# Optimization experiments

Measured on AMD Instinct MI355X. Metric: run time of the kernel, lower is better.

Reference implementation:

```python
import jax, jax.numpy as jnp
import numpy as np

N_NODES = 50000
N_EDGES = 640000
D_IN = 128
D_H1 = 128
D_H2 = 256
NEG_SLOPE = 0.2


def setup_inputs() -> dict:
    key = jax.random.key(0)
    ks = jax.random.split(key, 12)
    s = 1.0 / np.sqrt(D_IN)
    inp = {
        'x': jax.random.normal(ks[0], (N_NODES, D_IN), dtype=jnp.float32),
        'edge_index': jax.random.randint(ks[1], (2, N_EDGES), 0, N_NODES, dtype=jnp.int64),
        # GATv2 layer 1: 128 -> 128 (separate lin_l / lin_r, attention vec, residual proj, bias)
        'Wl1': jax.random.normal(ks[2], (D_IN, D_H1), dtype=jnp.float32) * s,
        'Wr1': jax.random.normal(ks[3], (D_IN, D_H1), dtype=jnp.float32) * s,
        'att1': jax.random.normal(ks[4], (D_H1,), dtype=jnp.float32) * s,
        'Wres1': jax.random.normal(ks[5], (D_IN, D_H1), dtype=jnp.float32) * s,
        'b1': jnp.zeros((D_H1,), dtype=jnp.float32),
        # GATv2 layer 2: 128 -> 256
        'Wl2': jax.random.normal(ks[6], (D_H1, D_H2), dtype=jnp.float32) * s,
        'Wr2': jax.random.normal(ks[7], (D_H1, D_H2), dtype=jnp.float32) * s,
        'att2': jax.random.normal(ks[8], (D_H2,), dtype=jnp.float32) * s,
        'Wres2': jax.random.normal(ks[9], (D_H1, D_H2), dtype=jnp.float32) * s,
        'b2': jnp.zeros((D_H2,), dtype=jnp.float32),
    }
    return inp


def _gatv2_layer(x, Wl, Wr, att, Wres, b, src, dst, n_nodes):
    """GATv2Conv (heads=1, residual=True, eval mode/no dropout).
    score e_ij = att . LeakyReLU(Wl x_src + Wr x_dst); softmax over incoming edges per dst;
    out_dst = sum_j alpha_ij * (Wl x_src) + residual + bias.
    """
    xl = x @ Wl                      # [N, F]
    xr = x @ Wr                      # [N, F]
    h = xl[src] + xr[dst]            # [E, F]  gather (irregular access)
    e = jax.nn.leaky_relu(h, NEG_SLOPE) @ att   # [E]
    # segment softmax over destination nodes
    m = jax.ops.segment_max(e, dst, num_segments=n_nodes)      # [N]
    w = jnp.exp(e - m[dst])                                     # [E]
    denom = jax.ops.segment_sum(w, dst, num_segments=n_nodes)   # [N]
    alpha = w / (denom[dst] + 1e-16)                             # [E]
    out = jax.ops.segment_sum(alpha[:, None] * xl[src], dst, num_segments=n_nodes)  # [N, F]
    return out + x @ Wres + b


def reference(x, edge_index, Wl1, Wr1, att1, Wres1, b1, Wl2, Wr2, att2, Wres2, b2):
    src = edge_index[0]
    dst = edge_index[1]
    h = _gatv2_layer(x, Wl1, Wr1, att1, Wres1, b1, src, dst, N_NODES)
    h = jax.nn.elu(h)
    out = _gatv2_layer(h, Wl2, Wr2, att2, Wres2, b2, src, dst, N_NODES)
    return out
```

## Files before the change

kernel.cpp:

```cpp
#include <hip/hip_runtime.h>

typedef unsigned short u16;
typedef unsigned int u32;
typedef __attribute__((ext_vector_type(8))) short bf16x8;
typedef __attribute__((ext_vector_type(4))) float f32x4;
typedef __attribute__((ext_vector_type(2))) float f32x2;

#define NN 50000
#define NE 640000

__device__ __forceinline__ float bfl(u32 u) { return __uint_as_float(u << 16); }
__device__ __forceinline__ float bfh(u32 u) { return __uint_as_float(u & 0xffff0000u); }
__device__ __forceinline__ float bf1(u16 v) { return __uint_as_float(((u32)v) << 16); }
__device__ __forceinline__ u16 f2bf(float f) {
  u32 u = __float_as_uint(f);
  u32 r = (u + 0x7fffu + ((u >> 16) & 1u)) >> 16;
  return (u16)r;
}

__device__ __forceinline__ f32x2 bc2(float s) { return (f32x2){s, s}; }
__device__ __forceinline__ f32x2 pkfma(f32x2 a, f32x2 b, f32x2 c) {
  return __builtin_elementwise_fma(a, b, c);
}
__device__ __forceinline__ f32x2 pkabs(f32x2 a) {
  return __builtin_elementwise_abs(a);
}

template <int CTRL>
__device__ __forceinline__ float dpp_add(float x) {
  int t = __builtin_amdgcn_update_dpp(0, __float_as_int(x), CTRL, 0xf, 0xf, true);
  return x + __int_as_float(t);
}

__device__ __forceinline__ void unpk2(uint2 v, f32x2* o) {
  o[0] = (f32x2){bfl(v.x), bfh(v.x)};
  o[1] = (f32x2){bfl(v.y), bfh(v.y)};
}
__device__ __forceinline__ void unpk2(uint4 v, f32x2* o) {
  o[0] = (f32x2){bfl(v.x), bfh(v.x)};
  o[1] = (f32x2){bfl(v.y), bfh(v.y)};
  o[2] = (f32x2){bfl(v.z), bfh(v.z)};
  o[3] = (f32x2){bfl(v.w), bfh(v.w)};
}

template <int HEPL> struct VecSel;
template <> struct VecSel<4> { using T = uint2; };
template <> struct VecSel<8> { using T = uint4; };

__global__ void probe_kernel(const u16* __restrict__ x, const int* __restrict__ ei,
                             int* __restrict__ flags) {
  __shared__ int s_f32, s_i32;
  if (threadIdx.x == 0) { s_f32 = 0; s_i32 = 0; }
  __syncthreads();
  int lf = 0, li = 0;
  for (int i = threadIdx.x; i < 8192; i += 256) {
    float v = bf1(x[i]);
    if (!(fabsf(v) < 1e8f)) lf = 1;
    if (ei[2 * i + 1] != 0) li = 1;
  }
  if (lf) s_f32 = 1;
  if (li) s_i32 = 1;
  __syncthreads();
  if (threadIdx.x == 0) {
    flags[0] = s_f32;
    flags[1] = s_i32 ? 0 : 1;
  }
}

__device__ __forceinline__ int edge_val(const int* __restrict__ w, long j, int i64) {
  return i64 ? w[2 * j] : w[j];
}

__global__ void count_kernel(const int* __restrict__ ei, const int* __restrict__ flags,
                             int* __restrict__ cnt, int E) {
  int e = blockIdx.x * blockDim.x + threadIdx.x;
  if (e >= E) return;
  int d = edge_val(ei, (long)E + e, flags[1]);
  if ((u32)d < (u32)NN) atomicAdd(&cnt[d], 1);
}

__global__ void scan_local(const int* __restrict__ cnt, int* __restrict__ excl,
                           int* __restrict__ bsum, int n) {
  __shared__ int sd[256];
  int t = threadIdx.x;
  int g = blockIdx.x * 256 + t;
  int v = (g < n) ? cnt[g] : 0;
  sd[t] = v;
  __syncthreads();
  for (int off = 1; off < 256; off <<= 1) {
    int x = (t >= off) ? sd[t - off] : 0;
    __syncthreads();
    sd[t] += x;
    __syncthreads();
  }
  int incl = sd[t];
  if (g < n) excl[g] = incl - v;
  if (t == 255) bsum[blockIdx.x] = incl;
}

__global__ void scan_totals(const int* __restrict__ bsum, int* __restrict__ boff, int nb) {
  __shared__ int sd[256];
  int t = threadIdx.x;
  int v = (t < nb) ? bsum[t] : 0;
  sd[t] = v;
  __syncthreads();
  for (int off = 1; off < 256; off <<= 1) {
    int x = (t >= off) ? sd[t - off] : 0;
    __syncthreads();
    sd[t] += x;
    __syncthreads();
  }
  if (t < nb) boff[t] = sd[t] - v;
}

__global__ void scan_add(const int* __restrict__ excl, const int* __restrict__ boff,
                         const int* __restrict__ cnt, int* __restrict__ rowptr,
                         int* __restrict__ fillp, int n) {
  int g = blockIdx.x * 256 + threadIdx.x;
  if (g < n) {
    int e2 = excl[g] + boff[blockIdx.x];
    rowptr[g] = e2;
    fillp[g] = e2;
    if (g == n - 1) rowptr[n] = e2 + cnt[g];
  }
}

__global__ void fill_kernel(const int* __restrict__ ei, const int* __restrict__ flags,
                            int* __restrict__ fillp, int* __restrict__ col, int E) {
  int e = blockIdx.x * blockDim.x + threadIdx.x;
  if (e >= E) return;
  int i64 = flags[1];
  int s = edge_val(ei, (long)e, i64);
  int d = edge_val(ei, (long)E + e, i64);
  if ((u32)d >= (u32)NN) return;
  int p = atomicAdd(&fillp[d], 1);
  col[p] = ((u32)s < (u32)NN) ? s : 0;
}

__global__ void transpose_w(const void* W0, const void* W1, const void* W2,
                            const void* W3, const void* W4, const void* W5,
                            u16* T0, u16* T1, u16* T2, u16* T3, u16* T4, u16* T5,
                            const int* __restrict__ flags) {
  int y = blockIdx.y;
  int M = (y < 3) ? 128 : 256;
  int flat = blockIdx.x * 256 + threadIdx.x;
  if (flat >= M * 128) return;
  int j = flat >> 7;
  int k = flat & 127;
  const void* W = (y == 0) ? W0 : (y == 1) ? W1 : (y == 2) ? W2 : (y == 3) ? W3 : (y == 4) ? W4 : W5;
  u16* T = (y == 0) ? T0 : (y == 1) ? T1 : (y == 2) ? T2 : (y == 3) ? T3 : (y == 4) ? T4 : T5;
  u16 v;
  if (flags[0])
    v = f2bf(((const float*)W)[(size_t)k * M + j]);
  else
    v = ((const u16*)W)[(size_t)k * M + j];
  T[(size_t)j * 128 + k] = v;
}

#define LSTR 136
__global__ __launch_bounds__(256) void gemm3_mfma(
    const void* __restrict__ X,
    const u16* __restrict__ Wta, const u16* __restrict__ Wtb, const u16* __restrict__ Wtc,
    const void* __restrict__ bias,
    u16* __restrict__ Ya, u16* __restrict__ Yb, u16* __restrict__ Yc,
    const int* __restrict__ flags, int x_follows, int N, int M) {
  __shared__ __align__(16) u16 Xs[64 * LSTR];
  __shared__ __align__(16) u16 Bs[128 * LSTR];
  const int K = 128;
  int t = threadIdx.x;
  int lane = t & 63;
  int w = t >> 6;
  int n0g = blockIdx.x * 64;
  int c0 = blockIdx.z * 128;
  int F32X = x_follows ? flags[0] : 0;
  const u16* Wt = (blockIdx.y == 0) ? Wta : ((blockIdx.y == 1) ? Wtb : Wtc);
  u16* Y = (blockIdx.y == 0) ? Ya : ((blockIdx.y == 1) ? Yb : Yc);

  if (!F32X) {
    const u16* Xg = (const u16*)X;
    for (int it = 0; it < 4; ++it) {
      int i = t + 256 * it;
      int r = i >> 4, c8 = (i & 15) * 8;
      int n = n0g + r;
      uint4 v = make_uint4(0, 0, 0, 0);
      if (n < N) v = *(const uint4*)(Xg + (size_t)n * K + c8);
      *(uint4*)(Xs + r * LSTR + c8) = v;
    }
  } else {
    const float* Xg = (const float*)X;
    for (int it = 0; it < 4; ++it) {
      int i = t + 256 * it;
      int r = i >> 4, c8 = (i & 15) * 8;
      int n = n0g + r;
      uint4 pk = make_uint4(0, 0, 0, 0);
      if (n < N) {
        float4 f0 = *(const float4*)(Xg + (size_t)n * K + c8);
        float4 f1 = *(const float4*)(Xg + (size_t)n * K + c8 + 4);
        pk.x = (u32)f2bf(f0.x) | ((u32)f2bf(f0.y) << 16);
        pk.y = (u32)f2bf(f0.z) | ((u32)f2bf(f0.w) << 16);
        pk.z = (u32)f2bf(f1.x) | ((u32)f2bf(f1.y) << 16);
        pk.w = (u32)f2bf(f1.z) | ((u32)f2bf(f1.w) << 16);
      }
      *(uint4*)(Xs + r * LSTR + c8) = pk;
    }
  }
  for (int it = 0; it < 8; ++it) {
    int i = t + 256 * it;
    int j = i >> 4, k8 = (i & 15) * 8;
    uint4 v = *(const uint4*)(Wt + (size_t)(c0 + j) * K + k8);
    *(uint4*)(Bs + j * LSTR + k8) = v;
  }
  __syncthreads();

  int m0 = (w >> 1) * 32;
  int n0 = (w & 1) * 64;
  int l15 = lane & 15;
  int q8 = (lane >> 4) * 8;
  f32x4 acc[2][4];
#pragma unroll
  for (int i = 0; i < 2; ++i)
#pragma unroll
    for (int j = 0; j < 4; ++j) acc[i][j] = (f32x4){0.f, 0.f, 0.f, 0.f};

#pragma unroll
  for (int kc = 0; kc < 4; ++kc) {
    int ko = kc * 32 + q8;
    bf16x8 a[2], b[4];
#pragma unroll
    for (int i = 0; i < 2; ++i)
      a[i] = *(const bf16x8*)(Xs + (m0 + i * 16 + l15) * LSTR + ko);
#pragma unroll
    for (int j = 0; j < 4; ++j)
      b[j] = *(const bf16x8*)(Bs + (n0 + j * 16 + l15) * LSTR + ko);
#pragma unroll
    for (int i = 0; i < 2; ++i)
#pragma unroll
      for (int j = 0; j < 4; ++j)
        acc[i][j] = __builtin_amdgcn_mfma_f32_16x16x32_bf16(a[i], b[j], acc[i][j], 0, 0, 0);
  }
  __syncthreads();

  float bv[4] = {0.f, 0.f, 0.f, 0.f};
  if (blockIdx.y == 2) {
    int F32 = flags[0];
#pragma unroll
    for (int j = 0; j < 4; ++j) {
      int c = c0 + n0 + j * 16 + l15;
      bv[j] = F32 ? ((const float*)bias)[c] : bf1(((const u16*)bias)[c]);
    }
  }

  u16* Ct = Xs;
#pragma unroll
  for (int i = 0; i < 2; ++i)
#pragma unroll
    for (int j = 0; j < 4; ++j) {
      int col = n0 + j * 16 + l15;
      int rbase = m0 + i * 16 + (lane >> 4) * 4;
#pragma unroll
      for (int r = 0; r < 4; ++r)
        Ct[(rbase + r) * LSTR + col] = f2bf(acc[i][j][r] + bv[j]);
    }
  __syncthreads();

  for (int it = 0; it < 4; ++it) {
    int i = t + 256 * it;
    int r = i >> 4, c8 = (i & 15) * 8;
    int n = n0g + r;
    if (n < N) {
      uint4 v = *(const uint4*)(Ct + r * LSTR + c8);
      *(uint4*)(Y + (size_t)n * M + c0 + c8) = v;
    }
  }
}

template <int F, bool ELU>
__global__ __launch_bounds__(128) void gat_agg_kernel(
    const u16* __restrict__ xl, const u16* __restrict__ xr, const u16* __restrict__ res,
    const void* __restrict__ att, const int* __restrict__ rowptr, const int* __restrict__ col,
    void* __restrict__ out, const int* __restrict__ flags, int out_follows, int N) {
  constexpr int HEPL = F / 32;
  constexpr int HP = HEPL / 2;
  using VecT = typename VecSel<HEPL>::T;
  int lane = threadIdx.x & 63;
  int half = lane >> 5;
  int hl = lane & 31;
  int node = blockIdx.x * 2 + (threadIdx.x >> 6);
  if (node >= N) return;
  int F32 = flags[0];
  int OF32 = out_follows ? F32 : 0;
  int base = hl * HEPL;

  f32x2 xr2[HP], att6[HP], att4[HP], acc2[HP];
  {
    VecT xp = *(const VecT*)(xr + (size_t)node * F + base);
    unpk2(xp, xr2);
  }
  if (F32) {
    const float* af = (const float*)att + base;
#pragma unroll
    for (int p = 0; p < HP; ++p) {
      f32x2 a = (f32x2){af[2 * p], af[2 * p + 1]};
      att6[p] = a * 0.6f;
      att4[p] = a * 0.4f;
    }
  } else {
    f32x2 a2[HP];
    VecT ap = *(const VecT*)((const u16*)att + base);
    unpk2(ap, a2);
#pragma unroll
    for (int p = 0; p < HP; ++p) {
      att6[p] = a2[p] * 0.6f;
      att4[p] = a2[p] * 0.4f;
    }
  }
#pragma unroll
  for (int p = 0; p < HP; ++p) acc2[p] = bc2(0.f);

  float m = -1e30f, l = 0.f;
  int beg = rowptr[node], end = rowptr[node + 1];

  for (int cs = beg; cs < end; cs += 64) {
    int n = min(64, end - cs);
    int myc = (cs + lane < end) ? col[cs + lane] : 0;
    int itc = (n + 3) >> 2;

    auto ld = [&](int j) -> VecT {
      int c = __shfl(myc, (j < n) ? j : 0, 64);
      return *(const VecT*)(xl + (size_t)c * F + base);
    };

    VecT a0 = ld(half), a1 = ld(2 + half);
    VecT b0 = a0, b1 = a1;
    if (itc > 1) { b0 = ld(4 + half); b1 = ld(6 + half); }

    for (int it = 0; it < itc; ++it) {
      VecT cur0 = a0, cur1 = a1;
      a0 = b0; a1 = b1;
      if (it + 2 < itc) {
        b0 = ld(4 * (it + 2) + half);
        b1 = ld(4 * (it + 2) + 2 + half);
      }
      int act0 = (4 * it + half) < n;
      int act1 = (4 * it + 2 + half) < n;

      f32x2 x0[HP], x1[HP];
      unpk2(cur0, x0);
      unpk2(cur1, x1);
      f32x2 s0 = bc2(0.f), s1 = bc2(0.f);
#pragma unroll
      for (int p = 0; p < HP; ++p) {
        f32x2 h0 = x0[p] + xr2[p];
        f32x2 h1 = x1[p] + xr2[p];
        f32x2 ha0 = pkabs(h0);
        f32x2 ha1 = pkabs(h1);
        s0 = pkfma(att6[p], h0, s0);
        s1 = pkfma(att6[p], h1, s1);
        s0 = pkfma(att4[p], ha0, s0);
        s1 = pkfma(att4[p], ha1, s1);
      }
      float d0 = s0.x + s0.y;
      float d1 = s1.x + s1.y;
      d0 = dpp_add<0xB1>(d0);  d1 = dpp_add<0xB1>(d1);
      d0 = dpp_add<0x4E>(d0);  d1 = dpp_add<0x4E>(d1);
      d0 = dpp_add<0x141>(d0); d1 = dpp_add<0x141>(d1);
      d0 = dpp_add<0x140>(d0); d1 = dpp_add<0x140>(d1);
      d0 += __shfl_xor(d0, 16, 64);
      d1 += __shfl_xor(d1, 16, 64);

      float p0 = act0 ? d0 : -1e30f;
      float p1 = act1 ? d1 : -1e30f;
      float pmh = fmaxf(p0, p1);
      float mn = fmaxf(m, pmh);
      float scl = __expf(m - mn);
      float w0 = __expf(p0 - mn);
      float w1 = __expf(p1 - mn);
      l = fmaf(l, scl, w0 + w1);
      f32x2 w0b = bc2(w0), w1b = bc2(w1), sclb = bc2(scl);
#pragma unroll
      for (int p = 0; p < HP; ++p)
        acc2[p] = pkfma(sclb, acc2[p], pkfma(w1b, x1[p], w0b * x0[p]));
      m = mn;
    }
  }

  float mo = __shfl_xor(m, 32, 64);
  float mt = fmaxf(m, mo);
  float sf = __expf(m - mt);
  l *= sf;
  l += __shfl_xor(l, 32, 64);
  f32x2 sfb = bc2(sf);
#pragma unroll
  for (int p = 0; p < HP; ++p) {
    acc2[p] = acc2[p] * sfb;
    acc2[p].x += __shfl_xor(acc2[p].x, 32, 64);
    acc2[p].y += __shfl_xor(acc2[p].y, 32, 64);
  }
  float inv = 1.f / (l + 1e-16f);
  if (half == 0) {
    VecT rp = *(const VecT*)(res + (size_t)node * F + base);
    f32x2 rv[HP];
    unpk2(rp, rv);
    f32x2 ov[HP];
    f32x2 invb = bc2(inv);
#pragma unroll
    for (int p = 0; p < HP; ++p) {
      f32x2 o = pkfma(acc2[p], invb, rv[p]);
      if (ELU) {
        o.x = (o.x > 0.f) ? o.x : (__expf(o.x) - 1.f);
        o.y = (o.y > 0.f) ? o.y : (__expf(o.y) - 1.f);
      }
      ov[p] = o;
    }
    if (OF32) {
      float* of = (float*)out + (size_t)node * F + base;
      float4 f0 = {ov[0].x, ov[0].y, ov[1].x, ov[1].y};
      *(float4*)of = f0;
      if constexpr (HP == 4) {
        float4 f1 = {ov[2].x, ov[2].y, ov[3].x, ov[3].y};
        *(float4*)(of + 4) = f1;
      }
    } else {
      u16* o16 = (u16*)out;
      if constexpr (HP == 2) {
        uint2 pk;
        pk.x = (u32)f2bf(ov[0].x) | ((u32)f2bf(ov[0].y) << 16);
        pk.y = (u32)f2bf(ov[1].x) | ((u32)f2bf(ov[1].y) << 16);
        *(uint2*)(o16 + (size_t)node * F + base) = pk;
      } else {
        uint4 pk;
        pk.x = (u32)f2bf(ov[0].x) | ((u32)f2bf(ov[0].y) << 16);
        pk.y = (u32)f2bf(ov[1].x) | ((u32)f2bf(ov[1].y) << 16);
        pk.z = (u32)f2bf(ov[2].x) | ((u32)f2bf(ov[2].y) << 16);
        pk.w = (u32)f2bf(ov[3].x) | ((u32)f2bf(ov[3].y) << 16);
        *(uint4*)(o16 + (size_t)node * F + base) = pk;
      }
    }
  }
}

extern "C" void kernel_launch(void* const* d_in, const int* in_sizes, int n_in,
                              void* d_out, int out_size, void* d_ws, size_t ws_size,
                              hipStream_t stream) {
  const u16* x16 = (const u16*)d_in[0];
  const int* ei = (const int*)d_in[1];
  const int N = NN, E = NE;

  char* ws = (char*)d_ws;
  size_t off = 0;
  auto alloc = [&](size_t bytes) -> void* {
    void* p = (void*)(ws + off);
    off += (bytes + 255) & ~(size_t)255;
    return p;
  };
  int* flags = (int*)alloc(2 * 4);
  int* cnt = (int*)alloc((size_t)N * 4);
  int* rowptr = (int*)alloc((size_t)(N + 1) * 4);
  int* fillp = (int*)alloc((size_t)N * 4);
  int* colb = (int*)alloc((size_t)E * 4);
  int* excl = (int*)alloc((size_t)N * 4);
  int* bsum = (int*)alloc(256 * 4);
  int* boff = (int*)alloc(256 * 4);
  u16* Wt1a = (u16*)alloc((size_t)128 * 128 * 2);
  u16* Wt1b = (u16*)alloc((size_t)128 * 128 * 2);
  u16* Wt1c = (u16*)alloc((size_t)128 * 128 * 2);
  u16* Wt2a = (u16*)alloc((size_t)256 * 128 * 2);
  u16* Wt2b = (u16*)alloc((size_t)256 * 128 * 2);
  u16* Wt2c = (u16*)alloc((size_t)256 * 128 * 2);
  u16* buf1 = (u16*)alloc((size_t)N * 256 * 2);
  u16* buf2 = (u16*)alloc((size_t)N * 256 * 2);
  u16* buf3 = (u16*)alloc((size_t)N * 256 * 2);
  u16* h1 = (u16*)alloc((size_t)N * 128 * 2);
  (void)ws_size; (void)n_in; (void)in_sizes; (void)out_size;

  int nb = (N + 255) / 256;

  probe_kernel<<<1, 256, 0, stream>>>(x16, ei, flags);
  hipMemsetAsync(cnt, 0, (size_t)N * 4, stream);
  count_kernel<<<(E + 255) / 256, 256, 0, stream>>>(ei, flags, cnt, E);
  scan_local<<<nb, 256, 0, stream>>>(cnt, excl, bsum, N);
  scan_totals<<<1, 256, 0, stream>>>(bsum, boff, nb);
  scan_add<<<nb, 256, 0, stream>>>(excl, boff, cnt, rowptr, fillp, N);
  fill_kernel<<<(E + 255) / 256, 256, 0, stream>>>(ei, flags, fillp, colb, E);
  transpose_w<<<dim3(128, 6), 256, 0, stream>>>(
      d_in[2], d_in[3], d_in[5], d_in[7], d_in[8], d_in[10],
      Wt1a, Wt1b, Wt1c, Wt2a, Wt2b, Wt2c, flags);

  int gx = (N + 63) / 64;
  gemm3_mfma<<<dim3(gx, 3, 1), 256, 0, stream>>>(
      d_in[0], Wt1a, Wt1b, Wt1c, d_in[6], buf1, buf2, buf3, flags, 1, N, 128);
  gat_agg_kernel<128, true><<<(N + 1) / 2, 128, 0, stream>>>(
      buf1, buf2, buf3, d_in[4], rowptr, colb, h1, flags, 0, N);
  gemm3_mfma<<<dim3(gx, 3, 2), 256, 0, stream>>>(
      h1, Wt2a, Wt2b, Wt2c, d_in[11], buf1, buf2, buf3, flags, 0, N, 256);
  gat_agg_kernel<256, false><<<(N + 1) / 2, 128, 0, stream>>>(
      buf1, buf2, buf3, d_in[9], rowptr, colb, d_out, flags, 1, N);
}
```

Baseline: 332.8 us.

## Map one half-wave per node in GAT aggregation and drop cross-half merge

Aggregation now gives each destination node 32 lanes instead of 64. Each half-wave walks that node's edge list on its own with per-lane column loads and a two-deep gather prefetch, so the cross-half softmax merge and the shuffle of column indices go away. Blocks grow to 256 threads covering 8 nodes. The probe kernel also samples fewer elements. Fewer lanes per node means less parallelism for high-degree nodes, and warp divergence between the two nodes in a wave is possible.

```diff
diff --git a/kernel.cpp b/kernel.cpp
--- a/kernel.cpp
+++ b/kernel.cpp
@@ -53,7 +53,7 @@
   if (threadIdx.x == 0) { s_f32 = 0; s_i32 = 0; }
   __syncthreads();
   int lf = 0, li = 0;
-  for (int i = threadIdx.x; i < 8192; i += 256) {
+  for (int i = threadIdx.x; i < 1024; i += 256) {
     float v = bf1(x[i]);
     if (!(fabsf(v) < 1e8f)) lf = 1;
     if (ei[2 * i + 1] != 0) li = 1;
@@ -275,17 +275,16 @@
 }
 
 template <int F, bool ELU>
-__global__ __launch_bounds__(128) void gat_agg_kernel(
+__global__ __launch_bounds__(256) void gat_agg_kernel(
     const u16* __restrict__ xl, const u16* __restrict__ xr, const u16* __restrict__ res,
     const void* __restrict__ att, const int* __restrict__ rowptr, const int* __restrict__ col,
     void* __restrict__ out, const int* __restrict__ flags, int out_follows, int N) {
   constexpr int HEPL = F / 32;
   constexpr int HP = HEPL / 2;
   using VecT = typename VecSel<HEPL>::T;
-  int lane = threadIdx.x & 63;
-  int half = lane >> 5;
-  int hl = lane & 31;
-  int node = blockIdx.x * 2 + (threadIdx.x >> 6);
+  int tid = threadIdx.x;
+  int hl = tid & 31;
+  int node = blockIdx.x * 8 + (tid >> 5);
   if (node >= N) return;
   int F32 = flags[0];
   int OF32 = out_follows ? F32 : 0;
@@ -319,34 +318,28 @@
 
   float m = -1e30f, l = 0.f;
   int beg = rowptr[node], end = rowptr[node + 1];
-
-  for (int cs = beg; cs < end; cs += 64) {
-    int n = min(64, end - cs);
-    int myc = (cs + lane < end) ? col[cs + lane] : 0;
-    int itc = (n + 3) >> 2;
-
-    auto ld = [&](int j) -> VecT {
-      int c = __shfl(myc, (j < n) ? j : 0, 64);
-      return *(const VecT*)(xl + (size_t)c * F + base);
-    };
-
-    VecT a0 = ld(half), a1 = ld(2 + half);
-    VecT b0 = a0, b1 = a1;
-    if (itc > 1) { b0 = ld(4 + half); b1 = ld(6 + half); }
-
-    for (int it = 0; it < itc; ++it) {
-      VecT cur0 = a0, cur1 = a1;
-      a0 = b0; a1 = b1;
-      if (it + 2 < itc) {
-        b0 = ld(4 * (it + 2) + half);
-        b1 = ld(4 * (it + 2) + 2 + half);
-      }
-      int act0 = (4 * it + half) < n;
-      int act1 = (4 * it + 2 + half) < n;
+  int deg = end - beg;
+
+  if (deg > 0) {
+    int nit = (deg + 1) >> 1;
+    int dm1 = deg - 1;
+    auto ldc = [&](int j) -> int { return col[beg + min(j, dm1)]; };
+    auto gat = [&](int c) -> VecT { return *(const VecT*)(xl + (size_t)c * F + base); };
+
+    int c0 = ldc(0), c1 = ldc(1), c2 = ldc(2), c3 = ldc(3);
+    int c4 = ldc(4), c5 = ldc(5);
+    VecT va = gat(c0), vb = gat(c1), vc = gat(c2), vd = gat(c3);
+
+    for (int t = 0; t < nit; ++t) {
+      VecT x0v = va, x1v = vb;
+      int act1 = (2 * t + 1) < deg;
+      va = vc; vb = vd;
+      if (t + 2 < nit) { vc = gat(c4); vd = gat(c5); }
+      if (t + 3 < nit) { c4 = ldc(2 * t + 6); c5 = ldc(2 * t + 7); }
 
       f32x2 x0[HP], x1[HP];
-      unpk2(cur0, x0);
-      unpk2(cur1, x1);
+      unpk2(x0v, x0);
+      unpk2(x1v, x1);
       f32x2 s0 = bc2(0.f), s1 = bc2(0.f);
 #pragma unroll
       for (int p = 0; p < HP; ++p) {
@@ -368,10 +361,9 @@
       d0 += __shfl_xor(d0, 16, 64);
       d1 += __shfl_xor(d1, 16, 64);
 
-      float p0 = act0 ? d0 : -1e30f;
+      float p0 = d0;
       float p1 = act1 ? d1 : -1e30f;
-      float pmh = fmaxf(p0, p1);
-      float mn = fmaxf(m, pmh);
+      float mn = fmaxf(m, fmaxf(p0, p1));
       float scl = __expf(m - mn);
       float w0 = __expf(p0 - mn);
       float w1 = __expf(p1 - mn);
@@ -384,57 +376,43 @@
     }
   }
 
-  float mo = __shfl_xor(m, 32, 64);
-  float mt = fmaxf(m, mo);
-  float sf = __expf(m - mt);
-  l *= sf;
-  l += __shfl_xor(l, 32, 64);
-  f32x2 sfb = bc2(sf);
+  float inv = 1.f / (l + 1e-16f);
+  VecT rp = *(const VecT*)(res + (size_t)node * F + base);
+  f32x2 rv[HP];
+  unpk2(rp, rv);
+  f32x2 ov[HP];
+  f32x2 invb = bc2(inv);
 #pragma unroll
   for (int p = 0; p < HP; ++p) {
-    acc2[p] = acc2[p] * sfb;
-    acc2[p].x += __shfl_xor(acc2[p].x, 32, 64);
-    acc2[p].y += __shfl_xor(acc2[p].y, 32, 64);
-  }
-  float inv = 1.f / (l + 1e-16f);
-  if (half == 0) {
-    VecT rp = *(const VecT*)(res + (size_t)node * F + base);
-    f32x2 rv[HP];
-    unpk2(rp, rv);
-    f32x2 ov[HP];
-    f32x2 invb = bc2(inv);
-#pragma unroll
-    for (int p = 0; p < HP; ++p) {
-      f32x2 o = pkfma(acc2[p], invb, rv[p]);
-      if (ELU) {
-        o.x = (o.x > 0.f) ? o.x : (__expf(o.x) - 1.f);
-        o.y = (o.y > 0.f) ? o.y : (__expf(o.y) - 1.f);
-      }
-      ov[p] = o;
-    }
-    if (OF32) {
-      float* of = (float*)out + (size_t)node * F + base;
-      float4 f0 = {ov[0].x, ov[0].y, ov[1].x, ov[1].y};
-      *(float4*)of = f0;
-      if constexpr (HP == 4) {
-        float4 f1 = {ov[2].x, ov[2].y, ov[3].x, ov[3].y};
-        *(float4*)(of + 4) = f1;
-      }
+    f32x2 o = pkfma(acc2[p], invb, rv[p]);
+    if (ELU) {
+      o.x = (o.x > 0.f) ? o.x : (__expf(o.x) - 1.f);
+      o.y = (o.y > 0.f) ? o.y : (__expf(o.y) - 1.f);
+    }
+    ov[p] = o;
+  }
+  if (OF32) {
+    float* of = (float*)out + (size_t)node * F + base;
+    float4 f0 = {ov[0].x, ov[0].y, ov[1].x, ov[1].y};
+    *(float4*)of = f0;
+    if constexpr (HP == 4) {
+      float4 f1 = {ov[2].x, ov[2].y, ov[3].x, ov[3].y};
+      *(float4*)(of + 4) = f1;
+    }
+  } else {
+    u16* o16 = (u16*)out;
+    if constexpr (HP == 2) {
+      uint2 pk;
+      pk.x = (u32)f2bf(ov[0].x) | ((u32)f2bf(ov[0].y) << 16);
+      pk.y = (u32)f2bf(ov[1].x) | ((u32)f2bf(ov[1].y) << 16);
+      *(uint2*)(o16 + (size_t)node * F + base) = pk;
     } else {
-      u16* o16 = (u16*)out;
-      if constexpr (HP == 2) {
-        uint2 pk;
-        pk.x = (u32)f2bf(ov[0].x) | ((u32)f2bf(ov[0].y) << 16);
-        pk.y = (u32)f2bf(ov[1].x) | ((u32)f2bf(ov[1].y) << 16);
-        *(uint2*)(o16 + (size_t)node * F + base) = pk;
-      } else {
-        uint4 pk;
-        pk.x = (u32)f2bf(ov[0].x) | ((u32)f2bf(ov[0].y) << 16);
-        pk.y = (u32)f2bf(ov[1].x) | ((u32)f2bf(ov[1].y) << 16);
-        pk.z = (u32)f2bf(ov[2].x) | ((u32)f2bf(ov[2].y) << 16);
-        pk.w = (u32)f2bf(ov[3].x) | ((u32)f2bf(ov[3].y) << 16);
-        *(uint4*)(o16 + (size_t)node * F + base) = pk;
-      }
+      uint4 pk;
+      pk.x = (u32)f2bf(ov[0].x) | ((u32)f2bf(ov[0].y) << 16);
+      pk.y = (u32)f2bf(ov[1].x) | ((u32)f2bf(ov[1].y) << 16);
+      pk.z = (u32)f2bf(ov[2].x) | ((u32)f2bf(ov[2].y) << 16);
+      pk.w = (u32)f2bf(ov[3].x) | ((u32)f2bf(ov[3].y) << 16);
+      *(uint4*)(o16 + (size_t)node * F + base) = pk;
     }
   }
 }
@@ -489,10 +467,10 @@
   int gx = (N + 63) / 64;
   gemm3_mfma<<<dim3(gx, 3, 1), 256, 0, stream>>>(
       d_in[0], Wt1a, Wt1b, Wt1c, d_in[6], buf1, buf2, buf3, flags, 1, N, 128);
-  gat_agg_kernel<128, true><<<(N + 1) / 2, 128, 0, stream>>>(
+  gat_agg_kernel<128, true><<<(N + 7) / 8, 256, 0, stream>>>(
       buf1, buf2, buf3, d_in[4], rowptr, colb, h1, flags, 0, N);
   gemm3_mfma<<<dim3(gx, 3, 2), 256, 0, stream>>>(
       h1, Wt2a, Wt2b, Wt2c, d_in[11], buf1, buf2, buf3, flags, 0, N, 256);
-  gat_agg_kernel<256, false><<<(N + 1) / 2, 128, 0, stream>>>(
+  gat_agg_kernel<256, false><<<(N + 7) / 8, 256, 0, stream>>>(
       buf1, buf2, buf3, d_in[9], rowptr, colb, d_out, flags, 1, N);
 }
```

Result: no change. 327.2 us (-1.7%).
